# Performance work log

Hardware: AMD Instinct MI355X
Metric: run time of the kernel (lower is better)

The kernel has to match this reference:

```python
import jax, jax.numpy as jnp
from jax import lax
import numpy as np

L, H, IN = 8, 32, 4      # num_layers, hidden_size, input_size
B, S = 1024, 512         # batch, seq_len
ODE_STEPS = 40           # fixed-step dopri5 substeps over t in [0, 60]
EPS = 1e-5               # BatchNorm eps

# physics constants (GRU.__init__ defaults)
CCAP, C_L, LAI, R_B = 1000.0, 2450.0, 2.6, 150.0
C_R, G_V, P_AIR, C_P_AIR, T_TOT, A2 = 1e-4, 0.3, 1.225, 1005.0, 0.7, 5.0


def setup_inputs() -> dict:
    key = jax.random.key(0)
    ks = jax.random.split(key, 24)
    p = lambda k, shape: 0.01 * jax.random.normal(k, shape, dtype=jnp.float32)
    return {
        'input_seq': jax.random.normal(ks[0], (B, S, IN), dtype=jnp.float32),
        'max_v': jax.random.uniform(ks[1], (4,), dtype=jnp.float32),
        'min_v': jax.random.uniform(ks[2], (4,), dtype=jnp.float32),
        # per-layer stacked params, torch Linear stored as [in, out] (y = x @ W + b)
        'Wr_w': p(ks[3], (L, IN, H)), 'Wr_b': p(ks[4], (L, H)),
        'Ur_w': p(ks[5], (L, H, H)),  'Ur_b': p(ks[6], (L, H)),
        'Wz_w': p(ks[7], (L, IN, H)), 'Wz_b': p(ks[8], (L, H)),
        'Uz_w': p(ks[9], (L, H, H)),  'Uz_b': p(ks[10], (L, H)),
        'Wh_w': p(ks[11], (L, IN, H)), 'Wh_b': p(ks[12], (L, H)),
        'Uh_w': p(ks[13], (L, H, H)),  'Uh_b': p(ks[14], (L, H)),
        'out_w': p(ks[15], (L, H, 4)), 'out_b': p(ks[16], (L, 4)),
        'bn_g': jnp.ones((L,), dtype=jnp.float32),   # BatchNorm1d(1) gamma per layer
        'bn_b': jnp.zeros((L,), dtype=jnp.float32),  # BatchNorm1d(1) beta per layer
    }


def reference(input_seq, max_v, min_v, Wr_w, Wr_b, Ur_w, Ur_b, Wz_w, Wz_b,
              Uz_w, Uz_b, Wh_w, Wh_b, Uh_w, Uh_b, out_w, out_b, bn_g, bn_b):
    b = input_seq.shape[0]
    h = jnp.zeros((b, H), dtype=input_seq.dtype)
    xs = jnp.swapaxes(input_seq, 0, 1)  # [S, B, IN]
    outs = None
    for l in range(L):  # hidden state is carried ACROSS layers as in the torch code
        Wr, br, Ur, bur = Wr_w[l], Wr_b[l], Ur_w[l], Ur_b[l]
        Wz, bz, Uz, buz = Wz_w[l], Wz_b[l], Uz_w[l], Uz_b[l]
        Wh, bh, Uh, buh = Wh_w[l], Wh_b[l], Uh_w[l], Uh_b[l]
        Wo, bo, g, bt = out_w[l], out_b[l], bn_g[l], bn_b[l]

        def cell(hc, x):
            r = jax.nn.sigmoid(x @ Wr + br + hc @ Ur + bur)
            z = jax.nn.sigmoid(x @ Wz + bz + hc @ Uz + buz)
            pre = x @ Wh + bh + r * (hc @ Uh + buh)  # [B, H]
            # BatchNorm1d(1) in train mode: single channel -> stats over all B*H elems
            m = pre.mean()
            v = jnp.mean((pre - m) ** 2)
            prop = jax.nn.relu((pre - m) / jnp.sqrt(v + EPS) * g + bt)
            hn = (1.0 - z) * hc + z * prop
            return hn, hn @ Wo + bo  # out [B, 4]

        h, outs = lax.scan(cell, h, xs)  # only last layer's outs survive, as in torch

    outs = jnp.transpose(outs, (1, 0, 2))  # [B, S, 4]
    den = outs * (max_v - min_v) + min_v
    Irad, Tout, Hair, Tair = den[..., 0], den[..., 1], den[..., 2], den[..., 3]

    Qsun = 10.0 * T_TOT * Irad
    Rn = 0.86 * (1.0 - jnp.exp(jnp.asarray(-0.7 * LAI, dtype=jnp.float32))) * Qsun

    def dydt(Ta):
        Ta = jnp.minimum(Ta, 500.0)
        Qcov = A2 * (Ta - Tout)
        Hair_sat = 5.5638 * jnp.exp(0.0572 * Ta)
        c_e = 0.7584 * jnp.exp(0.0518 * Ta)
        r_s = (82.0 + 570.0 * jnp.exp(-C_R * (Rn / LAI))) * (1.0 + 0.023 * (Ta - 5.0) ** 2)
        g_e = 2.0 * LAI / ((1.0 + c_e) * R_B + r_s)
        Hcrop = Hair_sat + c_e * R_B / (2.0 * LAI) * (Rn / C_L)
        Qtrans = g_e * (-C_L) * (Hcrop - Hair)
        Qvent = -(G_V * P_AIR * C_P_AIR) * (Ta - Tout)
        return (-1.0 / CCAP) * (Qsun - Qcov - Qtrans - Qvent)

    hs = 60.0 / ODE_STEPS  # fixed-step Dormand-Prince RK45

    def rk45(y, _):
        k1 = dydt(y)
        k2 = dydt(y + hs * (k1 / 5.0))
        k3 = dydt(y + hs * (3.0 / 40.0 * k1 + 9.0 / 40.0 * k2))
        k4 = dydt(y + hs * (44.0 / 45.0 * k1 - 56.0 / 15.0 * k2 + 32.0 / 9.0 * k3))
        k5 = dydt(y + hs * (19372.0 / 6561.0 * k1 - 25360.0 / 2187.0 * k2
                            + 64448.0 / 6561.0 * k3 - 212.0 / 729.0 * k4))
        k6 = dydt(y + hs * (9017.0 / 3168.0 * k1 - 355.0 / 33.0 * k2
                            + 46732.0 / 5247.0 * k3 + 49.0 / 176.0 * k4
                            - 5103.0 / 18656.0 * k5))
        yn = y + hs * (35.0 / 384.0 * k1 + 500.0 / 1113.0 * k3 + 125.0 / 192.0 * k4
                       - 2187.0 / 6784.0 * k5 + 11.0 / 84.0 * k6)
        return yn, None

    Tair_f, _ = lax.scan(rk45, Tair, None, length=ODE_STEPS)
    out = jnp.stack([Irad, Tout, Hair], axis=2)  # [B, S, 3]
    return Tair_f, out, Tair_f
```

## Files before the change

kernel.cpp:

```cpp
#include <hip/hip_runtime.h>
#include <math.h>

#define NL 8
#define SS 512
#define NBROWS 1024
#define NH 32
#define EPSV 1e-5f
#define BS (NBROWS*SS)
#define NBLK 64
#define RPT 2
#define RPB 16
#define FXS 16777216.0f
#define FXI (1.0/16777216.0)
#define GSTRIDE 16

#define ADD_TAG ((1ull<<52) + (1ull<<45))
#define SUB_TAG ((64ull<<52) + (64ull<<45))

__global__ void zero_ws(unsigned int* __restrict__ f, int n) {
    int i = blockIdx.x * blockDim.x + threadIdx.x;
    if (i < n) f[i] = 0u;
}

__global__ __launch_bounds__(256)
void gru_kernel(const float* __restrict__ xin,
                const float* __restrict__ maxv, const float* __restrict__ minv,
                const float* __restrict__ Wr_w, const float* __restrict__ Wr_b,
                const float* __restrict__ Ur_w, const float* __restrict__ Ur_b,
                const float* __restrict__ Wz_w, const float* __restrict__ Wz_b,
                const float* __restrict__ Uz_w, const float* __restrict__ Uz_b,
                const float* __restrict__ Wh_w, const float* __restrict__ Wh_b,
                const float* __restrict__ Uh_w, const float* __restrict__ Uh_b,
                const float* __restrict__ out_w, const float* __restrict__ out_b,
                const float* __restrict__ bn_g, const float* __restrict__ bn_b,
                float* __restrict__ dout,
                unsigned long long* __restrict__ gsum)
{
    const int tid  = threadIdx.x;
    const int j    = tid & 31;
    const int rg   = tid >> 5;
    const int lane = tid & 63;
    const int wid  = tid >> 6;
    const int bid  = blockIdx.x;

    __shared__ float hls[RPB][36];
    __shared__ float partials[4][2];
    __shared__ float bcast[2];

    float myh[RPT];
#pragma unroll
    for (int q = 0; q < RPT; ++q) { hls[rg + 8*q][j] = 0.f; myh[q] = 0.f; }
    __syncthreads();

    const float dv0 = maxv[0]-minv[0], dv1 = maxv[1]-minv[1];
    const float dv2 = maxv[2]-minv[2], dv3 = maxv[3]-minv[3];
    const float mv0 = minv[0], mv1 = minv[1], mv2 = minv[2], mv3 = minv[3];

    for (int l = 0; l < NL; ++l) {
        float ur[NH], uz[NH], uh[NH];
#pragma unroll
        for (int k = 0; k < NH; ++k) {
            ur[k] = Ur_w[(l*NH + k)*NH + j];
            uz[k] = Uz_w[(l*NH + k)*NH + j];
            uh[k] = Uh_w[(l*NH + k)*NH + j];
        }
        float wr[4], wz[4], wh[4];
#pragma unroll
        for (int i = 0; i < 4; ++i) {
            wr[i] = Wr_w[(l*4 + i)*NH + j];
            wz[i] = Wz_w[(l*4 + i)*NH + j];
            wh[i] = Wh_w[(l*4 + i)*NH + j];
        }
        const float brj = Wr_b[l*NH + j] + Ur_b[l*NH + j];
        const float bzj = Wz_b[l*NH + j] + Uz_b[l*NH + j];
        const float bhx = Wh_b[l*NH + j];
        const float bhu = Uh_b[l*NH + j];
        const float wo0 = out_w[(l*NH + j)*4 + 0];
        const float wo1 = out_w[(l*NH + j)*4 + 1];
        const float wo2 = out_w[(l*NH + j)*4 + 2];
        const float wo3 = out_w[(l*NH + j)*4 + 3];
        const float bo0 = out_b[l*4 + 0], bo1 = out_b[l*4 + 1];
        const float bo2 = out_b[l*4 + 2], bo3 = out_b[l*4 + 3];
        const float gg = bn_g[l], bb = bn_b[l];

        for (int s = 0; s < SS; ++s) {
            const int g = l*SS + s;
            float pre[RPT], zz[RPT];
            float s1 = 0.f, s2 = 0.f;
#pragma unroll
            for (int q = 0; q < RPT; ++q) {
                const int r    = rg + 8*q;
                const int brow = bid*RPB + r;
                const float4 xc = *(const float4*)&xin[(brow*SS + s)*4];
                float ar = brj, az = bzj, ax = bhx, au = bhu;
                const float4* hp = (const float4*)(&hls[r][0]);
#pragma unroll
                for (int kk = 0; kk < 8; ++kk) {
                    const float4 hv = hp[kk];
                    ar += hv.x*ur[4*kk+0]; az += hv.x*uz[4*kk+0]; au += hv.x*uh[4*kk+0];
                    ar += hv.y*ur[4*kk+1]; az += hv.y*uz[4*kk+1]; au += hv.y*uh[4*kk+1];
                    ar += hv.z*ur[4*kk+2]; az += hv.z*uz[4*kk+2]; au += hv.z*uh[4*kk+2];
                    ar += hv.w*ur[4*kk+3]; az += hv.w*uz[4*kk+3]; au += hv.w*uh[4*kk+3];
                }
                ar += xc.x*wr[0] + xc.y*wr[1] + xc.z*wr[2] + xc.w*wr[3];
                az += xc.x*wz[0] + xc.y*wz[1] + xc.z*wz[2] + xc.w*wz[3];
                ax += xc.x*wh[0] + xc.y*wh[1] + xc.z*wh[2] + xc.w*wh[3];
                const float rr = 1.f/(1.f + expf(-ar));
                zz[q]  = 1.f/(1.f + expf(-az));
                pre[q] = ax + rr*au;
                s1 += pre[q];
                s2 += pre[q]*pre[q];
            }
#pragma unroll
            for (int m = 1; m < 64; m <<= 1) {
                s1 += __shfl_xor(s1, m, 64);
                s2 += __shfl_xor(s2, m, 64);
            }
            if (lane == 0) { partials[wid][0] = s1; partials[wid][1] = s2; }
            __syncthreads();

            if (tid == 0) {
                const float b1 = partials[0][0] + partials[1][0] + partials[2][0] + partials[3][0];
                const float b2 = partials[0][1] + partials[1][1] + partials[2][1] + partials[3][1];
                const long long q1 = llrintf(b1 * FXS);
                const long long q2 = llrintf(b2 * FXS);
                atomicAdd(&gsum[(size_t)g*GSTRIDE + 0], ADD_TAG + (unsigned long long)q1);
                atomicAdd(&gsum[(size_t)g*GSTRIDE + 1], ADD_TAG + (unsigned long long)q2);
            }

            if (wid == 0) {
                unsigned long long u1, u2;
                for (;;) {
                    u1 = __hip_atomic_load(&gsum[(size_t)g*GSTRIDE + 0], __ATOMIC_RELAXED,
                                           __HIP_MEMORY_SCOPE_AGENT);
                    u2 = __hip_atomic_load(&gsum[(size_t)g*GSTRIDE + 1], __ATOMIC_RELAXED,
                                           __HIP_MEMORY_SCOPE_AGENT);
                    if ((u1 >> 52) >= NBLK && (u2 >> 52) >= NBLK) break;
                    __builtin_amdgcn_s_sleep(1);
                }
                const float t1 = (float)((double)(long long)(u1 - SUB_TAG) * FXI);
                const float t2 = (float)((double)(long long)(u2 - SUB_TAG) * FXI);
                const float mean = t1 * (1.f/32768.f);
                const float var  = t2 * (1.f/32768.f) - mean*mean;
                const float rstd = rsqrtf(var + EPSV);
                if (lane == 0) { bcast[0] = mean; bcast[1] = rstd; }
            }
            __syncthreads();
            const float mean = bcast[0], rstd = bcast[1];

#pragma unroll
            for (int q = 0; q < RPT; ++q) {
                const float prop = fmaxf((pre[q] - mean)*rstd*gg + bb, 0.f);
                const float hn   = (1.f - zz[q])*myh[q] + zz[q]*prop;
                myh[q] = hn;
                hls[rg + 8*q][j] = hn;
                if (l == NL - 1) {
                    float t0 = hn*wo0, t1o = hn*wo1, t2o = hn*wo2, t3o = hn*wo3;
#pragma unroll
                    for (int m = 1; m < 32; m <<= 1) {
                        t0  += __shfl_xor(t0,  m, 32);
                        t1o += __shfl_xor(t1o, m, 32);
                        t2o += __shfl_xor(t2o, m, 32);
                        t3o += __shfl_xor(t3o, m, 32);
                    }
                    if (j == 0) {
                        const int brow = bid*RPB + rg + 8*q;
                        const int idx  = brow*SS + s;
                        dout[BS + idx*3 + 0] = (t0  + bo0)*dv0 + mv0;
                        dout[BS + idx*3 + 1] = (t1o + bo1)*dv1 + mv1;
                        dout[BS + idx*3 + 2] = (t2o + bo2)*dv2 + mv2;
                        dout[idx]            = (t3o + bo3)*dv3 + mv3;
                    }
                }
            }
            __syncthreads();
        }
    }
}

__device__ __forceinline__ float dydt_f(float Ta, float Tout, float Hair,
                                        float Qsun, float Rn, float rsbase) {
    Ta = fminf(Ta, 500.f);
    const float Qcov = 5.f*(Ta - Tout);
    const float Hs   = 5.5638f*expf(0.0572f*Ta);
    const float ce   = 0.7584f*expf(0.0518f*Ta);
    const float dd   = Ta - 5.f;
    const float rs   = rsbase*(1.f + 0.023f*dd*dd);
    const float ge   = 5.2f/((1.f + ce)*150.f + rs);
    const float Hcrop  = Hs + ce*(150.f/5.2f)*(Rn/2450.f);
    const float Qtrans = ge*(-2450.f)*(Hcrop - Hair);
    const float Qvent  = -369.3375f*(Ta - Tout);
    return (-1.0f/1000.f)*(Qsun - Qcov - Qtrans - Qvent);
}

__global__ void ode_kernel(float* __restrict__ dout) {
    const int idx = blockIdx.x*blockDim.x + threadIdx.x;
    if (idx >= BS) return;
    float Ta = dout[idx];
    const float Irad = dout[BS + idx*3 + 0];
    const float Tout = dout[BS + idx*3 + 1];
    const float Hair = dout[BS + idx*3 + 2];
    const float Qsun = 7.f*Irad;
    const float Rn   = 0.86f*(1.f - expf(-1.82f))*Qsun;
    const float rsbase = 82.f + 570.f*expf(-1e-4f*(Rn/2.6f));
    const float hs = 1.5f;
#pragma unroll 1
    for (int it = 0; it < 40; ++it) {
        const float k1 = dydt_f(Ta, Tout, Hair, Qsun, Rn, rsbase);
        const float k2 = dydt_f(Ta + hs*(0.2f*k1), Tout, Hair, Qsun, Rn, rsbase);
        const float k3 = dydt_f(Ta + hs*(0.075f*k1 + 0.225f*k2), Tout, Hair, Qsun, Rn, rsbase);
        const float k4 = dydt_f(Ta + hs*((44.f/45.f)*k1 - (56.f/15.f)*k2 + (32.f/9.f)*k3),
                                Tout, Hair, Qsun, Rn, rsbase);
        const float k5 = dydt_f(Ta + hs*((19372.f/6561.f)*k1 - (25360.f/2187.f)*k2
                                         + (64448.f/6561.f)*k3 - (212.f/729.f)*k4),
                                Tout, Hair, Qsun, Rn, rsbase);
        const float k6 = dydt_f(Ta + hs*((9017.f/3168.f)*k1 - (355.f/33.f)*k2
                                         + (46732.f/5247.f)*k3 + (49.f/176.f)*k4
                                         - (5103.f/18656.f)*k5),
                                Tout, Hair, Qsun, Rn, rsbase);
        Ta = Ta + hs*((35.f/384.f)*k1 + (500.f/1113.f)*k3 + (125.f/192.f)*k4
                      - (2187.f/6784.f)*k5 + (11.f/84.f)*k6);
    }
    dout[idx] = Ta;
    dout[4*BS + idx] = Ta;
}

extern "C" void kernel_launch(void* const* d_in, const int* in_sizes, int n_in,
                              void* d_out, int out_size, void* d_ws, size_t ws_size,
                              hipStream_t stream) {
    const float* xin   = (const float*)d_in[0];
    const float* maxv  = (const float*)d_in[1];
    const float* minv  = (const float*)d_in[2];
    const float* Wr_w  = (const float*)d_in[3];
    const float* Wr_b  = (const float*)d_in[4];
    const float* Ur_w  = (const float*)d_in[5];
    const float* Ur_b  = (const float*)d_in[6];
    const float* Wz_w  = (const float*)d_in[7];
    const float* Wz_b  = (const float*)d_in[8];
    const float* Uz_w  = (const float*)d_in[9];
    const float* Uz_b  = (const float*)d_in[10];
    const float* Wh_w  = (const float*)d_in[11];
    const float* Wh_b  = (const float*)d_in[12];
    const float* Uh_w  = (const float*)d_in[13];
    const float* Uh_b  = (const float*)d_in[14];
    const float* out_w = (const float*)d_in[15];
    const float* out_b = (const float*)d_in[16];
    const float* bn_g  = (const float*)d_in[17];
    const float* bn_b  = (const float*)d_in[18];
    float* dout = (float*)d_out;

    const int steps = NL*SS;
    unsigned long long* gsum = (unsigned long long*)d_ws;
    const int nwords = steps*GSTRIDE*2;

    zero_ws<<<(nwords + 255)/256, 256, 0, stream>>>((unsigned int*)d_ws, nwords);

    gru_kernel<<<NBLK, 256, 0, stream>>>(xin, maxv, minv,
        Wr_w, Wr_b, Ur_w, Ur_b, Wz_w, Wz_b, Uz_w, Uz_b,
        Wh_w, Wh_b, Uh_w, Uh_b, out_w, out_b, bn_g, bn_b,
        dout, gsum);

    ode_kernel<<<BS/256, 256, 0, stream>>>(dout);
}
```

Baseline: 14.63 ms.

## Replace contended atomic-add barrier with per-block tagged slots and wave reduction

The per-step cross-block BatchNorm reduction no longer has all 64 blocks atomically add into one shared counter word. Each block now stores its quantized partial sums, tagged with the step number, into its own slot in a double-buffered array. Wave 0 of every block polls all 64 slots in parallel, one per lane, and reduces them with shuffles. This removes atomic contention on a single address and shrinks the workspace-zeroing kernel, but every block now polls 64 cache lines each step and spins without sleeping. Slot reuse relies on the two-deep buffer plus step tags for correctness.

```diff
diff --git a/kernel.cpp b/kernel.cpp
--- a/kernel.cpp
+++ b/kernel.cpp
@@ -12,10 +12,8 @@
 #define RPB 16
 #define FXS 16777216.0f
 #define FXI (1.0/16777216.0)
-#define GSTRIDE 16
-
-#define ADD_TAG ((1ull<<52) + (1ull<<45))
-#define SUB_TAG ((64ull<<52) + (64ull<<45))
+#define VBIAS (1ll<<49)
+#define VMASK ((1ull<<51)-1)
 
 __global__ void zero_ws(unsigned int* __restrict__ f, int n) {
     int i = blockIdx.x * blockDim.x + threadIdx.x;
@@ -34,7 +32,7 @@
                 const float* __restrict__ out_w, const float* __restrict__ out_b,
                 const float* __restrict__ bn_g, const float* __restrict__ bn_b,
                 float* __restrict__ dout,
-                unsigned long long* __restrict__ gsum)
+                unsigned long long* __restrict__ gslot)
 {
     const int tid  = threadIdx.x;
     const int j    = tid & 31;
@@ -119,29 +117,39 @@
             if (lane == 0) { partials[wid][0] = s1; partials[wid][1] = s2; }
             __syncthreads();
 
+            const unsigned long long tagw = ((unsigned long long)(g + 1)) << 51;
+
             if (tid == 0) {
                 const float b1 = partials[0][0] + partials[1][0] + partials[2][0] + partials[3][0];
                 const float b2 = partials[0][1] + partials[1][1] + partials[2][1] + partials[3][1];
                 const long long q1 = llrintf(b1 * FXS);
                 const long long q2 = llrintf(b2 * FXS);
-                atomicAdd(&gsum[(size_t)g*GSTRIDE + 0], ADD_TAG + (unsigned long long)q1);
-                atomicAdd(&gsum[(size_t)g*GSTRIDE + 1], ADD_TAG + (unsigned long long)q2);
+                unsigned long long* slot = &gslot[(((size_t)(g & 1))*NBLK + bid)*2];
+                __hip_atomic_store(&slot[0], tagw | (unsigned long long)(q1 + VBIAS),
+                                   __ATOMIC_RELAXED, __HIP_MEMORY_SCOPE_AGENT);
+                __hip_atomic_store(&slot[1], tagw | (unsigned long long)(q2 + VBIAS),
+                                   __ATOMIC_RELAXED, __HIP_MEMORY_SCOPE_AGENT);
             }
 
             if (wid == 0) {
+                const unsigned long long* sp = &gslot[(((size_t)(g & 1))*NBLK + lane)*2];
                 unsigned long long u1, u2;
                 for (;;) {
-                    u1 = __hip_atomic_load(&gsum[(size_t)g*GSTRIDE + 0], __ATOMIC_RELAXED,
-                                           __HIP_MEMORY_SCOPE_AGENT);
-                    u2 = __hip_atomic_load(&gsum[(size_t)g*GSTRIDE + 1], __ATOMIC_RELAXED,
-                                           __HIP_MEMORY_SCOPE_AGENT);
-                    if ((u1 >> 52) >= NBLK && (u2 >> 52) >= NBLK) break;
-                    __builtin_amdgcn_s_sleep(1);
-                }
-                const float t1 = (float)((double)(long long)(u1 - SUB_TAG) * FXI);
-                const float t2 = (float)((double)(long long)(u2 - SUB_TAG) * FXI);
-                const float mean = t1 * (1.f/32768.f);
-                const float var  = t2 * (1.f/32768.f) - mean*mean;
+                    u1 = __hip_atomic_load(&sp[0], __ATOMIC_RELAXED, __HIP_MEMORY_SCOPE_AGENT);
+                    u2 = __hip_atomic_load(&sp[1], __ATOMIC_RELAXED, __HIP_MEMORY_SCOPE_AGENT);
+                    const bool ready = ((u1 >> 51) == (unsigned long long)(g + 1)) &&
+                                       ((u2 >> 51) == (unsigned long long)(g + 1));
+                    if (__all(ready)) break;
+                }
+                float v1 = (float)((double)((long long)(u1 & VMASK) - VBIAS) * FXI);
+                float v2 = (float)((double)((long long)(u2 & VMASK) - VBIAS) * FXI);
+#pragma unroll
+                for (int m = 1; m < 64; m <<= 1) {
+                    v1 += __shfl_xor(v1, m, 64);
+                    v2 += __shfl_xor(v2, m, 64);
+                }
+                const float mean = v1 * (1.f/32768.f);
+                const float var  = v2 * (1.f/32768.f) - mean*mean;
                 const float rstd = rsqrtf(var + EPSV);
                 if (lane == 0) { bcast[0] = mean; bcast[1] = rstd; }
             }
@@ -249,16 +257,15 @@
     const float* bn_b  = (const float*)d_in[18];
     float* dout = (float*)d_out;
 
-    const int steps = NL*SS;
-    unsigned long long* gsum = (unsigned long long*)d_ws;
-    const int nwords = steps*GSTRIDE*2;
-
-    zero_ws<<<(nwords + 255)/256, 256, 0, stream>>>((unsigned int*)d_ws, nwords);
+    unsigned long long* gslot = (unsigned long long*)d_ws;
+    const int nwords = 2*NBLK*2*2;
+
+    zero_ws<<<1, 256, 0, stream>>>((unsigned int*)d_ws, nwords);
 
     gru_kernel<<<NBLK, 256, 0, stream>>>(xin, maxv, minv,
         Wr_w, Wr_b, Ur_w, Ur_b, Wz_w, Wz_b, Uz_w, Uz_b,
         Wh_w, Wh_b, Uh_w, Uh_b, out_w, out_b, bn_g, bn_b,
-        dout, gsum);
+        dout, gslot);
 
     ode_kernel<<<BS/256, 256, 0, stream>>>(dout);
 }
```

New measurement: 14.92 ms. 1.02x slower.

## Prefetch next-step inputs, spin without sleep, and drop trailing block barrier

Applied to the files above, without the earlier changes.

Loads the next timestep's input float4 into registers one step ahead, so the global load latency overlaps the recurrent matmul. The cross-block BatchNorm wait loop now polls continuously, with the next load issued before the check and no s_sleep, to shorten wake-up latency on the grid-wide reduction. The barrier at the end of each timestep is removed: each hidden-state row is written and read only by threads in the same wavefront, and the existing barriers already order the partials and broadcast buffers. Spinning without sleep raises memory traffic on the shared counters while blocks wait.

```diff
diff --git a/kernel.cpp b/kernel.cpp
--- a/kernel.cpp
+++ b/kernel.cpp
@@ -56,6 +56,11 @@
     const float dv2 = maxv[2]-minv[2], dv3 = maxv[3]-minv[3];
     const float mv0 = minv[0], mv1 = minv[1], mv2 = minv[2], mv3 = minv[3];
 
+    float4 xpre[RPT];
+#pragma unroll
+    for (int q = 0; q < RPT; ++q)
+        xpre[q] = *(const float4*)&xin[(((bid*RPB + rg + 8*q)*SS) + 0)*4];
+
     for (int l = 0; l < NL; ++l) {
         float ur[NH], uz[NH], uh[NH];
 #pragma unroll
@@ -85,13 +90,19 @@
 
         for (int s = 0; s < SS; ++s) {
             const int g = l*SS + s;
+
+            const int sn = (s + 1) & (SS - 1);
+            float4 xnew[RPT];
+#pragma unroll
+            for (int q = 0; q < RPT; ++q)
+                xnew[q] = *(const float4*)&xin[(((bid*RPB + rg + 8*q)*SS) + sn)*4];
+
             float pre[RPT], zz[RPT];
             float s1 = 0.f, s2 = 0.f;
 #pragma unroll
             for (int q = 0; q < RPT; ++q) {
-                const int r    = rg + 8*q;
-                const int brow = bid*RPB + r;
-                const float4 xc = *(const float4*)&xin[(brow*SS + s)*4];
+                const int r = rg + 8*q;
+                const float4 xc = xpre[q];
                 float ar = brj, az = bzj, ax = bhx, au = bhu;
                 const float4* hp = (const float4*)(&hls[r][0]);
 #pragma unroll
@@ -112,6 +123,9 @@
                 s2 += pre[q]*pre[q];
             }
 #pragma unroll
+            for (int q = 0; q < RPT; ++q) xpre[q] = xnew[q];
+
+#pragma unroll
             for (int m = 1; m < 64; m <<= 1) {
                 s1 += __shfl_xor(s1, m, 64);
                 s2 += __shfl_xor(s2, m, 64);
@@ -129,17 +143,17 @@
             }
 
             if (wid == 0) {
-                unsigned long long u1, u2;
+                const unsigned long long* sp = &gsum[(size_t)g*GSTRIDE];
+                unsigned long long a0 = __hip_atomic_load(&sp[0], __ATOMIC_RELAXED, __HIP_MEMORY_SCOPE_AGENT);
+                unsigned long long b0 = __hip_atomic_load(&sp[1], __ATOMIC_RELAXED, __HIP_MEMORY_SCOPE_AGENT);
                 for (;;) {
-                    u1 = __hip_atomic_load(&gsum[(size_t)g*GSTRIDE + 0], __ATOMIC_RELAXED,
-                                           __HIP_MEMORY_SCOPE_AGENT);
-                    u2 = __hip_atomic_load(&gsum[(size_t)g*GSTRIDE + 1], __ATOMIC_RELAXED,
-                                           __HIP_MEMORY_SCOPE_AGENT);
-                    if ((u1 >> 52) >= NBLK && (u2 >> 52) >= NBLK) break;
-                    __builtin_amdgcn_s_sleep(1);
+                    const unsigned long long a1 = __hip_atomic_load(&sp[0], __ATOMIC_RELAXED, __HIP_MEMORY_SCOPE_AGENT);
+                    const unsigned long long b1 = __hip_atomic_load(&sp[1], __ATOMIC_RELAXED, __HIP_MEMORY_SCOPE_AGENT);
+                    if (((a0 >> 52) >= NBLK) && ((b0 >> 52) >= NBLK)) break;
+                    a0 = a1; b0 = b1;
                 }
-                const float t1 = (float)((double)(long long)(u1 - SUB_TAG) * FXI);
-                const float t2 = (float)((double)(long long)(u2 - SUB_TAG) * FXI);
+                const float t1 = (float)((double)(long long)(a0 - SUB_TAG) * FXI);
+                const float t2 = (float)((double)(long long)(b0 - SUB_TAG) * FXI);
                 const float mean = t1 * (1.f/32768.f);
                 const float var  = t2 * (1.f/32768.f) - mean*mean;
                 const float rstd = rsqrtf(var + EPSV);
@@ -173,7 +187,6 @@
                     }
                 }
             }
-            __syncthreads();
         }
     }
 }
```

Measured after the change: 14.91 ms. About the same (+1.9%).
